# Optimization experiments

Measured on AMD Instinct MI355X. Metric: run time of the kernel, lower is better.

Reference implementation:

```python
import jax, jax.numpy as jnp
import numpy as np

B, T, K = 2, 2048, 1024
H, G = 16, 2          # heads, groups
HG = H // G            # kv heads = 8
KH = K // H            # head_dim = 64


def _rope(x, cos, sin):
    # x: (b, h, T, d); cos/sin: (T, d). Standard rotate-half RoPE.
    d2 = x.shape[-1] // 2
    x1, x2 = x[..., :d2], x[..., d2:]
    rot = jnp.concatenate([-x2, x1], axis=-1)
    return x * cos[None, None, :, :] + rot * sin[None, None, :, :]


def setup_inputs() -> dict:
    key = jax.random.key(0)
    k1, k2, k3 = jax.random.split(key, 3)
    x = jax.random.normal(k1, (B, T, K), dtype=jnp.float32)
    # weights stored as (in, out): y = x @ W
    w_qkv = jax.random.normal(k2, (K, K + 2 * K // G), dtype=jnp.float32) * (K ** -0.5)
    w_out = jax.random.normal(k3, (K, K), dtype=jnp.float32) * (K ** -0.5)
    # rotary tables
    inv_freq = 1.0 / (10000.0 ** (np.arange(0, KH, 2, dtype=np.float32) / KH))  # (KH/2,)
    ang = np.arange(T, dtype=np.float32)[:, None] * inv_freq[None, :]           # (T, KH/2)
    ang = np.concatenate([ang, ang], axis=-1)                                    # (T, KH)
    cos = jnp.asarray(np.cos(ang))
    sin = jnp.asarray(np.sin(ang))
    return {"x": x, "cos": cos, "sin": sin, "w_qkv": w_qkv, "w_out": w_out}


def reference(x, cos, sin, w_qkv, w_out):
    b, t, k = x.shape
    kv = k // G
    qkv = x @ w_qkv                                   # (b, T, k + 2*kv)
    Q = qkv[..., :k]
    Kt = qkv[..., k:k + kv]
    Vt = qkv[..., k + kv:]
    Q = Q.reshape(b, t, H, KH).transpose(0, 2, 1, 3)   # (b, H, T, KH)
    Kt = Kt.reshape(b, t, HG, KH).transpose(0, 2, 1, 3)  # (b, HG, T, KH)
    Vt = Vt.reshape(b, t, HG, KH).transpose(0, 2, 1, 3)
    # GQA head repeat: each kv head serves `groups` consecutive query heads
    Kt = jnp.repeat(Kt, G, axis=1)                     # (b, H, T, KH)
    Vt = jnp.repeat(Vt, G, axis=1)
    Q = _rope(Q, cos, sin)
    Kt = _rope(Kt, cos, sin)
    scores = jnp.einsum("bhqd,bhkd->bhqk", Q, Kt) * (KH ** -0.5)
    causal = jnp.tril(jnp.ones((t, t), dtype=bool))
    scores = jnp.where(causal[None, None], scores, jnp.finfo(scores.dtype).min)
    attn = jax.nn.softmax(scores, axis=-1)
    out = jnp.einsum("bhqk,bhkd->bhqd", attn, Vt)      # (b, H, T, KH)
    out = out.transpose(0, 2, 1, 3).reshape(b, t, k)
    return out @ w_out
```

## Files before the change

kernel.cpp:

```cpp
#include <hip/hip_runtime.h>

typedef unsigned short u16;
typedef unsigned int u32;
typedef short bf16x8 __attribute__((ext_vector_type(8)));
typedef float f32x4 __attribute__((ext_vector_type(4)));
typedef float f32x8v __attribute__((ext_vector_type(8)));
typedef float f32x16 __attribute__((ext_vector_type(16)));

#define LOG2E 1.44269504f

__device__ __forceinline__ u16 f2b(float f) {
  union { float f; unsigned u; } v; v.f = f;
  unsigned r = v.u + 0x7FFFu + ((v.u >> 16) & 1u);
  return (u16)(r >> 16);
}

__device__ __forceinline__ u32 pk2(float a, float b) {
  union { float f; u32 u; } x, y; x.f = a; y.f = b;
  return ((x.u + 0x8000u) >> 16) | ((y.u + 0x8000u) & 0xFFFF0000u);
}

__device__ __forceinline__ u32 cvtpk(float a, float b) {
  u32 r;
  asm("v_cvt_pk_bf16_f32 %0, %1, %2" : "=v"(r) : "v"(a), "v"(b));
  return r;
}

__device__ __forceinline__ float max3f(float a, float b, float c) {
  float r;
  asm("v_max3_f32 %0, %1, %2, %3" : "=v"(r) : "v"(a), "v"(b), "v"(c));
  return r;
}

__device__ __forceinline__ void plswap(u32& x, u32& y) {
#if __has_builtin(__builtin_amdgcn_permlane32_swap)
  typedef int v2i __attribute__((ext_vector_type(2)));
  v2i r = __builtin_amdgcn_permlane32_swap((int)x, (int)y, false, false);
  x = (u32)r[0]; y = (u32)r[1];
#else
  u32 sx = (u32)__shfl_xor((int)x, 32, 64);
  u32 sy = (u32)__shfl_xor((int)y, 32, 64);
  bool hi = (threadIdx.x & 63) >= 32;
  u32 nx = hi ? sy : x;
  u32 ny = hi ? y : sx;
  x = nx; y = ny;
#endif
}

__device__ __forceinline__ void gld16(const void* g, void* l) {
  __builtin_amdgcn_global_load_lds((const __attribute__((address_space(1))) void*)g,
                                   (__attribute__((address_space(3))) void*)l, 16, 0, 0);
}

__device__ __forceinline__ void invswz(int c, int& r, int& o) {
  int rhalf = c >> 3;
  int r2 = (rhalf >> 1) & 1;
  int r0 = ((c >> 2) & 1) ^ r2;
  r = rhalf * 2 + r0;
  int o0 = (c & 1) ^ r0;
  int o1 = ((c >> 1) & 1) ^ (rhalf & 1);
  o = o0 + 2 * o1;
}

__global__ __launch_bounds__(256) void k_prep0(const float* __restrict__ x, u16* __restrict__ Xb,
                                               const float* __restrict__ w_qkv, u16* __restrict__ Wqt,
                                               const float* __restrict__ w_out, u16* __restrict__ Wot) {
  __shared__ float tile[32][33];
  int blk = blockIdx.x;
  int tid = threadIdx.x;
  if (blk < 4096) {
    int i = blk * 256 + tid;
    float4 v = ((const float4*)x)[i];
    ushort4 o;
    o.x = f2b(v.x); o.y = f2b(v.y); o.z = f2b(v.z); o.w = f2b(v.w);
    ((ushort4*)Xb)[i] = o;
    return;
  }
  const float* in; u16* out; int R, C, t;
  if (blk < 6144) { t = blk - 4096; in = w_qkv; out = Wqt; R = 1024; C = 2048; }
  else            { t = blk - 6144; in = w_out; out = Wot; R = 1024; C = 1024; }
  int nbx = C >> 5;
  int c0 = (t % nbx) * 32, r0 = (t / nbx) * 32;
  int tx = tid & 31, ty = tid >> 5;
#pragma unroll
  for (int i = 0; i < 32; i += 8)
    tile[ty + i][tx] = in[(size_t)(r0 + ty + i) * C + c0 + tx];
  __syncthreads();
#pragma unroll
  for (int i = 0; i < 32; i += 8)
    out[(size_t)(c0 + ty + i) * R + r0 + tx] = f2b(tile[tx][ty + i]);
}

template<int BM, int Nsz, int Ksz, int EPI>
__global__ __launch_bounds__(256) void k_gemm(const u16* __restrict__ A, const u16* __restrict__ Bt,
                                              float* __restrict__ C, const float* __restrict__ cs,
                                              const float* __restrict__ sn, u16* __restrict__ Qb,
                                              u16* __restrict__ Kb, u16* __restrict__ Vt) {
  constexpr int MT = BM / 32;
  constexpr int CA = BM / 64;
  constexpr int ABytes = BM * 128;
  __shared__ u16 sm[(EPI == 1) ? 16640 : (BM * 64 + 8192)];
  const int tid = threadIdx.x;
  const int l = tid & 63, w = tid >> 6;
  const int wm = w >> 1, wn = w & 1;
  const int m0 = blockIdx.x * BM, n0 = blockIdx.y * 128;
  const int rg = l >> 4, cl = l & 15;

  const u16* aSrc[2];
  const u16* bSrc[2];
#pragma unroll
  for (int i = 0; i < CA; i++) {
    int r, o; invswz(i * 256 + tid, r, o);
    aSrc[i] = A + (size_t)(m0 + r) * Ksz + o * 8;
  }
#pragma unroll
  for (int i = 0; i < 2; i++) {
    int r, o; invswz(i * 256 + tid, r, o);
    bSrc[i] = Bt + (size_t)(n0 + r) * Ksz + o * 8;
  }

  auto stage = [&](int buf) {
#pragma unroll
    for (int i = 0; i < CA; i++) {
      gld16(aSrc[i], (char*)sm + buf * (BM * 64) + i * 4096 + w * 1024);
      aSrc[i] += 32;
    }
#pragma unroll
    for (int i = 0; i < 2; i++) {
      gld16(bSrc[i], (char*)sm + ABytes + buf * 8192 + i * 4096 + w * 1024);
      bSrc[i] += 32;
    }
  };

  f32x4 acc[MT][4] = {};
  const int NK = Ksz / 32;
  stage(0);
  for (int j = 0; j < NK; j++) {
    const int cur = j & 1;
    if (j + 1 < NK) {
      stage(cur ^ 1);
      if constexpr (CA == 2) asm volatile("s_waitcnt vmcnt(4)" ::: "memory");
      else                   asm volatile("s_waitcnt vmcnt(3)" ::: "memory");
    } else {
      asm volatile("s_waitcnt vmcnt(0)" ::: "memory");
    }
    __builtin_amdgcn_s_barrier();
    asm volatile("" ::: "memory");

    bf16x8 aF[MT], bF[4];
#pragma unroll
    for (int m = 0; m < MT; m++) {
      int row = wm * (BM / 2) + m * 16 + cl;
      unsigned ba = (unsigned)((row * 64 + rg * 16) ^ ((row & 7) << 4));
      aF[m] = *(const bf16x8*)((char*)sm + cur * (BM * 64) + ba);
    }
#pragma unroll
    for (int n = 0; n < 4; n++) {
      int row = wn * 64 + n * 16 + cl;
      unsigned ba = (unsigned)((row * 64 + rg * 16) ^ ((row & 7) << 4));
      bF[n] = *(const bf16x8*)((char*)sm + ABytes + cur * 8192 + ba);
    }
    __builtin_amdgcn_s_setprio(1);
#pragma unroll
    for (int m = 0; m < MT; m++)
#pragma unroll
      for (int n = 0; n < 4; n++)
        acc[m][n] = __builtin_amdgcn_mfma_f32_16x16x32_bf16(aF[m], bF[n], acc[m][n], 0, 0, 0);
    __builtin_amdgcn_s_setprio(0);
    asm volatile("" ::: "memory");
    __builtin_amdgcn_s_barrier();
  }

  if constexpr (EPI == 0) {
#pragma unroll
    for (int m = 0; m < MT; m++)
#pragma unroll
      for (int n = 0; n < 4; n++)
#pragma unroll
        for (int r = 0; r < 4; r++)
          C[(size_t)(m0 + wm * (BM / 2) + m * 16 + rg * 4 + r) * Nsz + n0 + wn * 64 + n * 16 + cl] =
              acc[m][n][r];
  } else {
    const int col0 = n0 + wn * 64;
    if (col0 < 1536) {
      const bool isQ = col0 < 1024;
      const float scale = isQ ? 0.125f : 1.0f;
      u16* dst = isQ ? Qb : Kb;
      const int hh = isQ ? (col0 >> 6) : ((col0 - 1024) >> 6);
      const int HN = isQ ? 16 : 8;
#pragma unroll
      for (int m = 0; m < MT; m++)
#pragma unroll
        for (int r = 0; r < 4; r++) {
          int tg = m0 + wm * (BM / 2) + m * 16 + rg * 4 + r;
          int bb = tg >> 11, tt = tg & 2047;
          size_t base = ((size_t)(bb * HN + hh) * 2048 + tt) * 64;
#pragma unroll
          for (int n = 0; n < 4; n++) {
            int d = n * 16 + cl;
            float cv = cs[tt * 64 + d], sv = sn[tt * 64 + d];
            float partner = acc[m][n ^ 2][r];
            float val = acc[m][n][r] * cv + ((n < 2) ? -partner : partner) * sv;
            dst[base + d] = f2b(val * scale);
          }
        }
    } else {
      __syncthreads();
      u16* tb = sm;
#pragma unroll
      for (int m = 0; m < MT; m++)
#pragma unroll
        for (int r = 0; r < 4; r++) {
          int tr = wm * (BM / 2) + m * 16 + rg * 4 + r;
#pragma unroll
          for (int n = 0; n < 4; n++)
            tb[tr * 130 + wn * 64 + n * 16 + cl] = f2b(acc[m][n][r]);
        }
      __syncthreads();
      const int bb = m0 >> 11, t0 = m0 & 2047;
#pragma unroll
      for (int i = 0; i < 32; i++) {
        int idx = i * 256 + tid;
        int d = idx >> 6, tp = (idx & 63) * 2;
        u32 v = (u32)tb[tp * 130 + d] | ((u32)tb[(tp + 1) * 130 + d] << 16);
        int dcol = n0 - 1536 + d;
        *(u32*)(Vt + (((size_t)(bb * 8) + (dcol >> 6)) * 64 + (dcol & 63)) * 2048 + t0 + tp) = v;
      }
    }
  }
}

__global__ __launch_bounds__(256, 4) void k_flash13(const u16* __restrict__ Qb, const u16* __restrict__ Kb,
                                                    const u16* __restrict__ Vt, u16* __restrict__ Ob) {
  __shared__ u16 smem[16384];
  const int tid = threadIdx.x;
  const int l = tid & 63, w = tid >> 6;
  const int sid = w >> 1;
  const int h01 = w & 1;
  const int bid = blockIdx.x;
  const int bkh = bid & 15;
  const int j = bid >> 4;
  const int qt = (j & 1) ? (63 - (j >> 1)) : (j >> 1);
  const int b = bkh >> 3, kh = bkh & 7;
  const int h = kh * 2 + h01;
  const int q0 = qt * 32;
  const int lq = l & 31, hi = l >> 5;
  const int q = q0 + lq;

  const int cnt = (qt + 2 - sid) >> 1;
  const int CNTMAX = (qt + 2) >> 1;

  const u16* Kg = Kb + (size_t)(b * 8 + kh) * 2048 * 64;
  const u16* Vg = Vt + (size_t)(b * 8 + kh) * 64 * 2048;
  const u16* Qp = Qb + ((size_t)(b * 16 + h) * 2048 + q) * 64 + hi * 8;

  const int krow = h01 * 16 + (l >> 3);
  const int swk1 = (krow ^ (krow >> 3)) & 7;
  const int swk2 = ((krow + 8) ^ ((krow + 8) >> 3)) & 7;
  const u16* kS1 = Kg + (size_t)(sid * 32 + krow) * 64 + (((l & 7) ^ swk1) << 3);
  const u16* kS2 = Kg + (size_t)(sid * 32 + krow + 8) * 64 + (((l & 7) ^ swk2) << 3);
  const int vd = h01 * 32 + (l >> 2);
  const int swv1 = ((vd >> 1) ^ (vd >> 3)) & 3;
  const int swv2 = (((vd + 16) >> 1) ^ ((vd + 16) >> 3)) & 3;
  const u16* vS0 = Vg + (size_t)vd * 2048 + sid * 32 + (((l & 3) ^ swv1) << 3);
  const u16* vS1 = Vg + (size_t)(vd + 16) * 2048 + sid * 32 + (((l & 3) ^ swv2) << 3);
  char* smB = (char*)smem;
  const int kDst = sid * 16384 + h01 * 2048;
  const int vDst = sid * 16384 + 8192 + h01 * 2048;

#define STAGE(buf)                                         \
  {                                                        \
    gld16(kS1, smB + kDst + (buf) * 4096);                 \
    gld16(kS2, smB + kDst + (buf) * 4096 + 1024);          \
    gld16(vS0, smB + vDst + (buf) * 4096);                 \
    gld16(vS1, smB + vDst + (buf) * 4096 + 1024);          \
    kS1 += 4096; kS2 += 4096; vS0 += 64; vS1 += 64;        \
  }

  if (cnt > 0) STAGE(0);

  bf16x8 qf[4];
#pragma unroll
  for (int ks = 0; ks < 4; ks++) qf[ks] = *(const bf16x8*)(Qp + ks * 16);

  union { u32 uu[4]; bf16x8 v; } ones;
#pragma unroll
  for (int jo = 0; jo < 4; jo++) ones.uu[jo] = 0x3F803F80u;

  f32x16 oa[2] = {};
  f32x16 lacc = {};
  float m = -3e38f;
  const int swzkr = (lq ^ (lq >> 3)) & 7;
  const int swzvr = ((lq >> 1) ^ (lq >> 3)) & 3;

  for (int i = 0; i < CNTMAX; i++) {
    const int cur = i & 1;
    asm volatile("s_waitcnt vmcnt(0)" ::: "memory");
    __builtin_amdgcn_s_barrier();
    asm volatile("" ::: "memory");
    if (i + 1 < cnt) STAGE(cur ^ 1);

    if (i < cnt) {
      const int t = sid + 2 * i;
      const char* KL = smB + sid * 16384 + cur * 4096;
      const char* VL = smB + sid * 16384 + 8192 + cur * 4096;

      bf16x8 kf[4];
#pragma unroll
      for (int ks = 0; ks < 4; ks++)
        kf[ks] = *(const bf16x8*)(KL + lq * 128 + ((((ks << 1) | hi) ^ swzkr) << 4));
      f32x16 s0 = {};
      __builtin_amdgcn_s_setprio(1);
#pragma unroll
      for (int ks = 0; ks < 4; ks++)
        s0 = __builtin_amdgcn_mfma_f32_32x32x16_bf16(kf[ks], qf[ks], s0, 0, 0, 0);
      __builtin_amdgcn_s_setprio(0);

      if (t == qt) {
#pragma unroll
        for (int r = 0; r < 16; r++) {
          int kvr = (t << 5) + (r & 3) + 8 * (r >> 2) + 4 * hi;
          if (kvr > q) s0[r] = -3e38f;
        }
      }

      float a5[5];
#pragma unroll
      for (int jo = 0; jo < 5; jo++) a5[jo] = max3f(s0[3 * jo], s0[3 * jo + 1], s0[3 * jo + 2]);
      float mx16 = fmaxf(max3f(a5[0], a5[1], a5[2]), max3f(a5[3], a5[4], s0[15]));
      bool keep = __all(mx16 - m <= 8.f);
      if (!keep) {
        float mx = fmaxf(mx16, __shfl_xor(mx16, 32, 64));
        float mnew = fmaxf(m, mx);
        float alpha = exp2f((m - mnew) * LOG2E);
        m = mnew;
        lacc[0] *= alpha;
#pragma unroll
        for (int r = 0; r < 16; r++) { oa[0][r] *= alpha; oa[1][r] *= alpha; }
      }
      float mb = m * LOG2E;
#pragma unroll
      for (int r = 0; r < 16; r++) s0[r] = exp2f(fmaf(s0[r], LOG2E, -mb));

      u32 aw[8];
#pragma unroll
      for (int jo = 0; jo < 8; jo++) aw[jo] = cvtpk(s0[2 * jo], s0[2 * jo + 1]);
      plswap(aw[0], aw[2]); plswap(aw[1], aw[3]);
      plswap(aw[4], aw[6]); plswap(aw[5], aw[7]);
      union { u32 uu[4]; bf16x8 v; } p0, p1;
#pragma unroll
      for (int jo = 0; jo < 4; jo++) { p0.uu[jo] = aw[jo]; p1.uu[jo] = aw[4 + jo]; }

      bf16x8 vf[2][2];
#pragma unroll
      for (int dt = 0; dt < 2; dt++)
#pragma unroll
        for (int p = 0; p < 2; p++)
          vf[dt][p] = *(const bf16x8*)(VL + (dt * 32 + lq) * 64 + ((((p << 1) | hi) ^ swzvr) << 4));

      __builtin_amdgcn_s_setprio(1);
#pragma unroll
      for (int dt = 0; dt < 2; dt++) {
        oa[dt] = __builtin_amdgcn_mfma_f32_32x32x16_bf16(vf[dt][0], p0.v, oa[dt], 0, 0, 0);
        oa[dt] = __builtin_amdgcn_mfma_f32_32x32x16_bf16(vf[dt][1], p1.v, oa[dt], 0, 0, 0);
      }
      lacc = __builtin_amdgcn_mfma_f32_32x32x16_bf16(ones.v, p0.v, lacc, 0, 0, 0);
      lacc = __builtin_amdgcn_mfma_f32_32x32x16_bf16(ones.v, p1.v, lacc, 0, 0, 0);
      __builtin_amdgcn_s_setprio(0);
    }
    asm volatile("" ::: "memory");
  }

  float lsum = lacc[0];

  __syncthreads();
  float* pbuf = (float*)smem;
  float* mlb = (float*)((char*)smem + 16896);
  u32* otileB = (u32*)((char*)smem + 17920);
  if (sid == 1) {
    float* pb = pbuf + (h01 * 64 + l) * 33;
#pragma unroll
    for (int r = 0; r < 16; r++) { pb[r] = oa[0][r]; pb[16 + r] = oa[1][r]; }
    mlb[h01 * 128 + l] = m;
    mlb[h01 * 128 + 64 + l] = lsum;
  }
  __syncthreads();
  if (sid == 0) {
    float m1 = mlb[h01 * 128 + l], l1 = mlb[h01 * 128 + 64 + l];
    float ms = fmaxf(m, m1);
    float a0 = exp2f((m - ms) * LOG2E);
    float a1 = exp2f((m1 - ms) * LOG2E);
    float linv = 1.0f / (lsum * a0 + l1 * a1);
    a0 *= linv; a1 *= linv;
    const float* pb = pbuf + (h01 * 64 + l) * 33;
    float of[32];
#pragma unroll
    for (int r = 0; r < 16; r++) {
      of[r] = oa[0][r] * a0 + pb[r] * a1;
      of[16 + r] = oa[1][r] * a0 + pb[16 + r] * a1;
    }
    u32* ot = otileB + h01 * (32 * 33);
#pragma unroll
    for (int dt = 0; dt < 2; dt++)
#pragma unroll
      for (int r = 0; r < 16; r += 2) {
        int d = dt * 32 + (r & 3) + 8 * (r >> 2) + 4 * hi;
        ot[lq * 33 + (d >> 1)] = cvtpk(of[dt * 16 + r], of[dt * 16 + r + 1]);
      }
#pragma unroll
    for (int i2 = 0; i2 < 16; i2++) {
      int wd = i2 * 64 + l;
      int row = wd >> 5, col = wd & 31;
      u32 v = ot[row * 33 + col];
      *(u32*)(Ob + (size_t)(b * 2048 + q0 + row) * 1024 + h * 64 + col * 2) = v;
    }
  }
#undef STAGE
}

extern "C" void kernel_launch(void* const* d_in, const int* in_sizes, int n_in,
                              void* d_out, int out_size, void* d_ws, size_t ws_size,
                              hipStream_t stream) {
  const float* x = (const float*)d_in[0];
  const float* cs = (const float*)d_in[1];
  const float* sn = (const float*)d_in[2];
  const float* w_qkv = (const float*)d_in[3];
  const float* w_out = (const float*)d_in[4];
  float* out = (float*)d_out;
  char* ws = (char*)d_ws;

  u16* Xb  = (u16*)(ws);
  u16* Wqt = (u16*)(ws + ((size_t)8u << 20));
  u16* Wot = (u16*)(ws + ((size_t)12u << 20));
  u16* Qb  = (u16*)(ws + ((size_t)18u << 20));
  u16* Kb  = (u16*)(ws + ((size_t)26u << 20));
  u16* Vt  = (u16*)(ws + ((size_t)30u << 20));
  u16* Ob  = (u16*)(ws + ((size_t)34u << 20));

  k_prep0<<<7168, 256, 0, stream>>>(x, Xb, w_qkv, Wqt, w_out, Wot);
  k_gemm<128, 2048, 1024, 1><<<dim3(32, 16), 256, 0, stream>>>(Xb, Wqt, nullptr, cs, sn, Qb, Kb, Vt);
  k_flash13<<<1024, 256, 0, stream>>>(Qb, Kb, Vt, Ob);
  k_gemm<64, 1024, 1024, 0><<<dim3(64, 8), 256, 0, stream>>>(Ob, Wot, out, nullptr, nullptr, nullptr, nullptr, nullptr);
}
```

Before: 101.3 us.

## Make flash attention persistent with atomic work queue and triple-buffered K/V

Converts the attention kernel into a persistent kernel with 768 blocks that fetch work units from a global atomic counter, processing the longest causal query tiles first for better load balance. It also deepens the K/V shared-memory pipeline from double to triple buffering, waiting on partial vmcnt so two tiles stay in flight. This raises shared memory per block and drops the occupancy hint in launch bounds. It also adds a memset and an atomic plus barrier per work unit.

```diff
diff --git a/kernel.cpp b/kernel.cpp
--- a/kernel.cpp
+++ b/kernel.cpp
@@ -13,11 +13,6 @@
   union { float f; unsigned u; } v; v.f = f;
   unsigned r = v.u + 0x7FFFu + ((v.u >> 16) & 1u);
   return (u16)(r >> 16);
-}
-
-__device__ __forceinline__ u32 pk2(float a, float b) {
-  union { float f; u32 u; } x, y; x.f = a; y.f = b;
-  return ((x.u + 0x8000u) >> 16) | ((y.u + 0x8000u) & 0xFFFF0000u);
 }
 
 __device__ __forceinline__ u32 cvtpk(float a, float b) {
@@ -230,192 +225,203 @@
   }
 }
 
-__global__ __launch_bounds__(256, 4) void k_flash13(const u16* __restrict__ Qb, const u16* __restrict__ Kb,
-                                                    const u16* __restrict__ Vt, u16* __restrict__ Ob) {
-  __shared__ u16 smem[16384];
+__global__ __launch_bounds__(256) void k_flash14(const u16* __restrict__ Qb, const u16* __restrict__ Kb,
+                                                 const u16* __restrict__ Vt, u16* __restrict__ Ob,
+                                                 u32* __restrict__ ctr) {
+  __shared__ u16 smem[24576];
+  __shared__ u32 sUnit;
   const int tid = threadIdx.x;
   const int l = tid & 63, w = tid >> 6;
   const int sid = w >> 1;
   const int h01 = w & 1;
-  const int bid = blockIdx.x;
-  const int bkh = bid & 15;
-  const int j = bid >> 4;
-  const int qt = (j & 1) ? (63 - (j >> 1)) : (j >> 1);
-  const int b = bkh >> 3, kh = bkh & 7;
-  const int h = kh * 2 + h01;
-  const int q0 = qt * 32;
   const int lq = l & 31, hi = l >> 5;
-  const int q = q0 + lq;
-
-  const int cnt = (qt + 2 - sid) >> 1;
-  const int CNTMAX = (qt + 2) >> 1;
-
-  const u16* Kg = Kb + (size_t)(b * 8 + kh) * 2048 * 64;
-  const u16* Vg = Vt + (size_t)(b * 8 + kh) * 64 * 2048;
-  const u16* Qp = Qb + ((size_t)(b * 16 + h) * 2048 + q) * 64 + hi * 8;
-
+  char* smB = (char*)smem;
+  const int kBase = sid * 24576 + h01 * 2048;
+  const int vBase = sid * 24576 + 12288 + h01 * 2048;
+  const int swzkr = (lq ^ (lq >> 3)) & 7;
+  const int swzvr = ((lq >> 1) ^ (lq >> 3)) & 3;
   const int krow = h01 * 16 + (l >> 3);
   const int swk1 = (krow ^ (krow >> 3)) & 7;
   const int swk2 = ((krow + 8) ^ ((krow + 8) >> 3)) & 7;
-  const u16* kS1 = Kg + (size_t)(sid * 32 + krow) * 64 + (((l & 7) ^ swk1) << 3);
-  const u16* kS2 = Kg + (size_t)(sid * 32 + krow + 8) * 64 + (((l & 7) ^ swk2) << 3);
   const int vd = h01 * 32 + (l >> 2);
   const int swv1 = ((vd >> 1) ^ (vd >> 3)) & 3;
   const int swv2 = (((vd + 16) >> 1) ^ ((vd + 16) >> 3)) & 3;
-  const u16* vS0 = Vg + (size_t)vd * 2048 + sid * 32 + (((l & 3) ^ swv1) << 3);
-  const u16* vS1 = Vg + (size_t)(vd + 16) * 2048 + sid * 32 + (((l & 3) ^ swv2) << 3);
-  char* smB = (char*)smem;
-  const int kDst = sid * 16384 + h01 * 2048;
-  const int vDst = sid * 16384 + 8192 + h01 * 2048;
+
+  union { u32 uu[4]; bf16x8 v; } ones;
+#pragma unroll
+  for (int jo = 0; jo < 4; jo++) ones.uu[jo] = 0x3F803F80u;
+
+  while (true) {
+    if (tid == 0) sUnit = atomicAdd(ctr, 1u);
+    __syncthreads();
+    const u32 u = sUnit;
+    if (u >= 1024u) break;
+
+    const int qt = 63 - (int)(u >> 4);
+    const int bkh = (int)(u & 15u);
+    const int b = bkh >> 3, kh = bkh & 7;
+    const int h = kh * 2 + h01;
+    const int q0 = qt * 32;
+    const int q = q0 + lq;
+
+    const int cnt = (qt + 2 - sid) >> 1;
+    const int CNTMAX = (qt + 2) >> 1;
+
+    const u16* Kg = Kb + (size_t)(b * 8 + kh) * 2048 * 64;
+    const u16* Vg = Vt + (size_t)(b * 8 + kh) * 64 * 2048;
+    const u16* Qp = Qb + ((size_t)(b * 16 + h) * 2048 + q) * 64 + hi * 8;
+
+    const u16* kS1 = Kg + (size_t)(sid * 32 + krow) * 64 + (((l & 7) ^ swk1) << 3);
+    const u16* kS2 = Kg + (size_t)(sid * 32 + krow + 8) * 64 + (((l & 7) ^ swk2) << 3);
+    const u16* vS0 = Vg + (size_t)vd * 2048 + sid * 32 + (((l & 3) ^ swv1) << 3);
+    const u16* vS1 = Vg + (size_t)(vd + 16) * 2048 + sid * 32 + (((l & 3) ^ swv2) << 3);
 
 #define STAGE(buf)                                         \
-  {                                                        \
-    gld16(kS1, smB + kDst + (buf) * 4096);                 \
-    gld16(kS2, smB + kDst + (buf) * 4096 + 1024);          \
-    gld16(vS0, smB + vDst + (buf) * 4096);                 \
-    gld16(vS1, smB + vDst + (buf) * 4096 + 1024);          \
-    kS1 += 4096; kS2 += 4096; vS0 += 64; vS1 += 64;        \
-  }
-
-  if (cnt > 0) STAGE(0);
-
-  bf16x8 qf[4];
-#pragma unroll
-  for (int ks = 0; ks < 4; ks++) qf[ks] = *(const bf16x8*)(Qp + ks * 16);
-
-  union { u32 uu[4]; bf16x8 v; } ones;
-#pragma unroll
-  for (int jo = 0; jo < 4; jo++) ones.uu[jo] = 0x3F803F80u;
-
-  f32x16 oa[2] = {};
-  f32x16 lacc = {};
-  float m = -3e38f;
-  const int swzkr = (lq ^ (lq >> 3)) & 7;
-  const int swzvr = ((lq >> 1) ^ (lq >> 3)) & 3;
-
-  for (int i = 0; i < CNTMAX; i++) {
-    const int cur = i & 1;
-    asm volatile("s_waitcnt vmcnt(0)" ::: "memory");
-    __builtin_amdgcn_s_barrier();
-    asm volatile("" ::: "memory");
-    if (i + 1 < cnt) STAGE(cur ^ 1);
-
-    if (i < cnt) {
-      const int t = sid + 2 * i;
-      const char* KL = smB + sid * 16384 + cur * 4096;
-      const char* VL = smB + sid * 16384 + 8192 + cur * 4096;
-
-      bf16x8 kf[4];
-#pragma unroll
-      for (int ks = 0; ks < 4; ks++)
-        kf[ks] = *(const bf16x8*)(KL + lq * 128 + ((((ks << 1) | hi) ^ swzkr) << 4));
-      f32x16 s0 = {};
-      __builtin_amdgcn_s_setprio(1);
-#pragma unroll
-      for (int ks = 0; ks < 4; ks++)
-        s0 = __builtin_amdgcn_mfma_f32_32x32x16_bf16(kf[ks], qf[ks], s0, 0, 0, 0);
-      __builtin_amdgcn_s_setprio(0);
-
-      if (t == qt) {
-#pragma unroll
-        for (int r = 0; r < 16; r++) {
-          int kvr = (t << 5) + (r & 3) + 8 * (r >> 2) + 4 * hi;
-          if (kvr > q) s0[r] = -3e38f;
-        }
+    {                                                      \
+      gld16(kS1, smB + kBase + (buf) * 4096);              \
+      gld16(kS2, smB + kBase + (buf) * 4096 + 1024);       \
+      gld16(vS0, smB + vBase + (buf) * 4096);              \
+      gld16(vS1, smB + vBase + (buf) * 4096 + 1024);       \
+      kS1 += 4096; kS2 += 4096; vS0 += 64; vS1 += 64;      \
+    }
+
+    if (cnt > 0) STAGE(0);
+    if (cnt > 1) STAGE(1);
+
+    bf16x8 qf[4];
+#pragma unroll
+    for (int ks = 0; ks < 4; ks++) qf[ks] = *(const bf16x8*)(Qp + ks * 16);
+
+    f32x16 oa[2] = {};
+    f32x16 lacc = {};
+    float m = -3e38f;
+    int cur = 0;
+
+    for (int i = 0; i < CNTMAX; i++) {
+      if (i + 1 < cnt) asm volatile("s_waitcnt vmcnt(4)" ::: "memory");
+      else             asm volatile("s_waitcnt vmcnt(0)" ::: "memory");
+      __builtin_amdgcn_s_barrier();
+      asm volatile("" ::: "memory");
+      if (i + 2 < cnt) STAGE(cur == 0 ? 2 : cur - 1);
+
+      if (i < cnt) {
+        const int t = sid + 2 * i;
+        const char* KL = smB + sid * 24576 + cur * 4096;
+        const char* VL = smB + sid * 24576 + 12288 + cur * 4096;
+
+        bf16x8 kf[4];
+#pragma unroll
+        for (int ks = 0; ks < 4; ks++)
+          kf[ks] = *(const bf16x8*)(KL + lq * 128 + ((((ks << 1) | hi) ^ swzkr) << 4));
+        f32x16 s0 = {};
+        __builtin_amdgcn_s_setprio(1);
+#pragma unroll
+        for (int ks = 0; ks < 4; ks++)
+          s0 = __builtin_amdgcn_mfma_f32_32x32x16_bf16(kf[ks], qf[ks], s0, 0, 0, 0);
+        __builtin_amdgcn_s_setprio(0);
+
+        if (t == qt) {
+#pragma unroll
+          for (int r = 0; r < 16; r++) {
+            int kvr = (t << 5) + (r & 3) + 8 * (r >> 2) + 4 * hi;
+            if (kvr > q) s0[r] = -3e38f;
+          }
+        }
+
+        float a5[5];
+#pragma unroll
+        for (int jo = 0; jo < 5; jo++) a5[jo] = max3f(s0[3 * jo], s0[3 * jo + 1], s0[3 * jo + 2]);
+        float mx16 = fmaxf(max3f(a5[0], a5[1], a5[2]), max3f(a5[3], a5[4], s0[15]));
+        bool keep = __all(mx16 - m <= 8.f);
+        if (!keep) {
+          float mx = fmaxf(mx16, __shfl_xor(mx16, 32, 64));
+          float mnew = fmaxf(m, mx);
+          float alpha = exp2f((m - mnew) * LOG2E);
+          m = mnew;
+          lacc[0] *= alpha;
+#pragma unroll
+          for (int r = 0; r < 16; r++) { oa[0][r] *= alpha; oa[1][r] *= alpha; }
+        }
+        float mb = m * LOG2E;
+#pragma unroll
+        for (int r = 0; r < 16; r++) s0[r] = exp2f(fmaf(s0[r], LOG2E, -mb));
+
+        u32 aw[8];
+#pragma unroll
+        for (int jo = 0; jo < 8; jo++) aw[jo] = cvtpk(s0[2 * jo], s0[2 * jo + 1]);
+        plswap(aw[0], aw[2]); plswap(aw[1], aw[3]);
+        plswap(aw[4], aw[6]); plswap(aw[5], aw[7]);
+        union { u32 uu[4]; bf16x8 v; } p0, p1;
+#pragma unroll
+        for (int jo = 0; jo < 4; jo++) { p0.uu[jo] = aw[jo]; p1.uu[jo] = aw[4 + jo]; }
+
+        bf16x8 vf[2][2];
+#pragma unroll
+        for (int dt = 0; dt < 2; dt++)
+#pragma unroll
+          for (int p = 0; p < 2; p++)
+            vf[dt][p] = *(const bf16x8*)(VL + (dt * 32 + lq) * 64 + ((((p << 1) | hi) ^ swzvr) << 4));
+
+        __builtin_amdgcn_s_setprio(1);
+#pragma unroll
+        for (int dt = 0; dt < 2; dt++) {
+          oa[dt] = __builtin_amdgcn_mfma_f32_32x32x16_bf16(vf[dt][0], p0.v, oa[dt], 0, 0, 0);
+          oa[dt] = __builtin_amdgcn_mfma_f32_32x32x16_bf16(vf[dt][1], p1.v, oa[dt], 0, 0, 0);
+        }
+        lacc = __builtin_amdgcn_mfma_f32_32x32x16_bf16(ones.v, p0.v, lacc, 0, 0, 0);
+        lacc = __builtin_amdgcn_mfma_f32_32x32x16_bf16(ones.v, p1.v, lacc, 0, 0, 0);
+        __builtin_amdgcn_s_setprio(0);
       }
-
-      float a5[5];
-#pragma unroll
-      for (int jo = 0; jo < 5; jo++) a5[jo] = max3f(s0[3 * jo], s0[3 * jo + 1], s0[3 * jo + 2]);
-      float mx16 = fmaxf(max3f(a5[0], a5[1], a5[2]), max3f(a5[3], a5[4], s0[15]));
-      bool keep = __all(mx16 - m <= 8.f);
-      if (!keep) {
-        float mx = fmaxf(mx16, __shfl_xor(mx16, 32, 64));
-        float mnew = fmaxf(m, mx);
-        float alpha = exp2f((m - mnew) * LOG2E);
-        m = mnew;
-        lacc[0] *= alpha;
-#pragma unroll
-        for (int r = 0; r < 16; r++) { oa[0][r] *= alpha; oa[1][r] *= alpha; }
+      cur = (cur == 2) ? 0 : cur + 1;
+      asm volatile("" ::: "memory");
+    }
+
+    float lsum = lacc[0];
+
+    __syncthreads();
+    float* pbuf = (float*)smem;
+    float* mlb = (float*)((char*)smem + 16896);
+    u32* otileB = (u32*)((char*)smem + 17920);
+    if (sid == 1) {
+      float* pb = pbuf + (h01 * 64 + l) * 33;
+#pragma unroll
+      for (int r = 0; r < 16; r++) { pb[r] = oa[0][r]; pb[16 + r] = oa[1][r]; }
+      mlb[h01 * 128 + l] = m;
+      mlb[h01 * 128 + 64 + l] = lsum;
+    }
+    __syncthreads();
+    if (sid == 0) {
+      float m1 = mlb[h01 * 128 + l], l1 = mlb[h01 * 128 + 64 + l];
+      float ms = fmaxf(m, m1);
+      float a0 = exp2f((m - ms) * LOG2E);
+      float a1 = exp2f((m1 - ms) * LOG2E);
+      float linv = 1.0f / (lsum * a0 + l1 * a1);
+      a0 *= linv; a1 *= linv;
+      const float* pb = pbuf + (h01 * 64 + l) * 33;
+      float of[32];
+#pragma unroll
+      for (int r = 0; r < 16; r++) {
+        of[r] = oa[0][r] * a0 + pb[r] * a1;
+        of[16 + r] = oa[1][r] * a0 + pb[16 + r] * a1;
       }
-      float mb = m * LOG2E;
-#pragma unroll
-      for (int r = 0; r < 16; r++) s0[r] = exp2f(fmaf(s0[r], LOG2E, -mb));
-
-      u32 aw[8];
-#pragma unroll
-      for (int jo = 0; jo < 8; jo++) aw[jo] = cvtpk(s0[2 * jo], s0[2 * jo + 1]);
-      plswap(aw[0], aw[2]); plswap(aw[1], aw[3]);
-      plswap(aw[4], aw[6]); plswap(aw[5], aw[7]);
-      union { u32 uu[4]; bf16x8 v; } p0, p1;
-#pragma unroll
-      for (int jo = 0; jo < 4; jo++) { p0.uu[jo] = aw[jo]; p1.uu[jo] = aw[4 + jo]; }
-
-      bf16x8 vf[2][2];
+      u32* ot = otileB + h01 * (32 * 33);
 #pragma unroll
       for (int dt = 0; dt < 2; dt++)
 #pragma unroll
-        for (int p = 0; p < 2; p++)
-          vf[dt][p] = *(const bf16x8*)(VL + (dt * 32 + lq) * 64 + ((((p << 1) | hi) ^ swzvr) << 4));
-
-      __builtin_amdgcn_s_setprio(1);
-#pragma unroll
-      for (int dt = 0; dt < 2; dt++) {
-        oa[dt] = __builtin_amdgcn_mfma_f32_32x32x16_bf16(vf[dt][0], p0.v, oa[dt], 0, 0, 0);
-        oa[dt] = __builtin_amdgcn_mfma_f32_32x32x16_bf16(vf[dt][1], p1.v, oa[dt], 0, 0, 0);
+        for (int r = 0; r < 16; r += 2) {
+          int d = dt * 32 + (r & 3) + 8 * (r >> 2) + 4 * hi;
+          ot[lq * 33 + (d >> 1)] = cvtpk(of[dt * 16 + r], of[dt * 16 + r + 1]);
+        }
+#pragma unroll
+      for (int i2 = 0; i2 < 16; i2++) {
+        int wd = i2 * 64 + l;
+        int row = wd >> 5, col = wd & 31;
+        u32 v = ot[row * 33 + col];
+        *(u32*)(Ob + (size_t)(b * 2048 + q0 + row) * 1024 + h * 64 + col * 2) = v;
       }
-      lacc = __builtin_amdgcn_mfma_f32_32x32x16_bf16(ones.v, p0.v, lacc, 0, 0, 0);
-      lacc = __builtin_amdgcn_mfma_f32_32x32x16_bf16(ones.v, p1.v, lacc, 0, 0, 0);
-      __builtin_amdgcn_s_setprio(0);
-    }
-    asm volatile("" ::: "memory");
-  }
-
-  float lsum = lacc[0];
-
-  __syncthreads();
-  float* pbuf = (float*)smem;
-  float* mlb = (float*)((char*)smem + 16896);
-  u32* otileB = (u32*)((char*)smem + 17920);
-  if (sid == 1) {
-    float* pb = pbuf + (h01 * 64 + l) * 33;
-#pragma unroll
-    for (int r = 0; r < 16; r++) { pb[r] = oa[0][r]; pb[16 + r] = oa[1][r]; }
-    mlb[h01 * 128 + l] = m;
-    mlb[h01 * 128 + 64 + l] = lsum;
-  }
-  __syncthreads();
-  if (sid == 0) {
-    float m1 = mlb[h01 * 128 + l], l1 = mlb[h01 * 128 + 64 + l];
-    float ms = fmaxf(m, m1);
-    float a0 = exp2f((m - ms) * LOG2E);
-    float a1 = exp2f((m1 - ms) * LOG2E);
-    float linv = 1.0f / (lsum * a0 + l1 * a1);
-    a0 *= linv; a1 *= linv;
-    const float* pb = pbuf + (h01 * 64 + l) * 33;
-    float of[32];
-#pragma unroll
-    for (int r = 0; r < 16; r++) {
-      of[r] = oa[0][r] * a0 + pb[r] * a1;
-      of[16 + r] = oa[1][r] * a0 + pb[16 + r] * a1;
-    }
-    u32* ot = otileB + h01 * (32 * 33);
-#pragma unroll
-    for (int dt = 0; dt < 2; dt++)
-#pragma unroll
-      for (int r = 0; r < 16; r += 2) {
-        int d = dt * 32 + (r & 3) + 8 * (r >> 2) + 4 * hi;
-        ot[lq * 33 + (d >> 1)] = cvtpk(of[dt * 16 + r], of[dt * 16 + r + 1]);
-      }
-#pragma unroll
-    for (int i2 = 0; i2 < 16; i2++) {
-      int wd = i2 * 64 + l;
-      int row = wd >> 5, col = wd & 31;
-      u32 v = ot[row * 33 + col];
-      *(u32*)(Ob + (size_t)(b * 2048 + q0 + row) * 1024 + h * 64 + col * 2) = v;
-    }
-  }
+    }
 #undef STAGE
+  }
 }
 
 extern "C" void kernel_launch(void* const* d_in, const int* in_sizes, int n_in,
@@ -436,9 +442,11 @@
   u16* Kb  = (u16*)(ws + ((size_t)26u << 20));
   u16* Vt  = (u16*)(ws + ((size_t)30u << 20));
   u16* Ob  = (u16*)(ws + ((size_t)34u << 20));
-
+  u32* ctr = (u32*)(ws + ((size_t)42u << 20));
+
+  hipMemsetAsync(ctr, 0, 4, stream);
   k_prep0<<<7168, 256, 0, stream>>>(x, Xb, w_qkv, Wqt, w_out, Wot);
   k_gemm<128, 2048, 1024, 1><<<dim3(32, 16), 256, 0, stream>>>(Xb, Wqt, nullptr, cs, sn, Qb, Kb, Vt);
-  k_flash13<<<1024, 256, 0, stream>>>(Qb, Kb, Vt, Ob);
+  k_flash14<<<768, 256, 0, stream>>>(Qb, Kb, Vt, Ob, ctr);
   k_gemm<64, 1024, 1024, 0><<<dim3(64, 8), 256, 0, stream>>>(Ob, Wot, out, nullptr, nullptr, nullptr, nullptr, nullptr);
 }
```

Result: slower. 122.9 us (+21.4%).
